# Optimization experiments

Hardware: AMD Instinct MI355X
Metric: run time of the kernel (lower is better)

## Reference

```python
import jax, jax.numpy as jnp
import numpy as np
import math


def _fft_size(n: int) -> int:
    return max(2 * 2 ** int(math.ceil(math.log2(n))), 16)


def setup_inputs() -> dict:
    key = jax.random.key(0)
    k1, k2 = jax.random.split(key)
    b, n, d = 4, 8192, 512
    x = jax.random.normal(k1, (b, n, d), dtype=jnp.float32)
    t = jax.random.normal(k2, (n, d), dtype=jnp.float32)
    return {"x": x, "t": t}


def reference(x, t):
    # x: (b, n, d); t: (n, d) Toeplitz coefficients t0..t_{n-1} per channel.
    # o[b, i, d] = gelu( sum_{j<=i} t[i-j, d] * x[b, j, d] )
    # computed via zero-padded real FFT of size >= 2n (causal linear conv).
    b, n, d = x.shape
    N = _fft_size(n)  # 2 * next_pow2(n)
    t_f = jnp.fft.rfft(t, n=N, axis=0)          # (N//2+1, d) complex
    x_f = jnp.fft.rfft(x, n=N, axis=1)          # (b, N//2+1, d) complex
    y = jnp.fft.irfft(x_f * t_f[None], n=N, axis=1)[:, :n, :]  # (b, n, d)
    return jax.nn.gelu(y)
```

## Files before the change

kernel.cpp:

```cpp
#include <hip/hip_runtime.h>
#include <hip/hip_bf16.h>

typedef short short8 __attribute__((ext_vector_type(8)));
typedef float f32x4  __attribute__((ext_vector_type(4)));

#define N_SEQ 8192
#define D_CH  512

constexpr int XSLOTS  = 2048;
constexpr int XLDS_B  = XSLOTS * 8;
constexpr int TSTRIDE = 272;
constexpr int TLDS_B  = 8 * TSTRIDE;
constexpr int ALL_LDS = XLDS_B + TLDS_B;

__device__ __forceinline__ unsigned short f32_to_bf16_bits(float f) {
    union { float f; unsigned int u; } v; v.f = f;
    unsigned int u = v.u;
    unsigned int r = u + 0x7FFFu + ((u >> 16) & 1u);
    return (unsigned short)(r >> 16);
}

__device__ __forceinline__ float gelu_f(float v) {
  float w = v * (2.3022031f + 0.10294296f * v * v);
  float e = __builtin_amdgcn_exp2f(w);
  float r = __builtin_amdgcn_rcpf(e + 1.0f);
  return v - v * r;
}

__global__ __launch_bounds__(256) void transpose_cast_kernel(
    const float* __restrict__ x, const float* __restrict__ t,
    unsigned short* __restrict__ xT, unsigned short* __restrict__ tT) {
  __shared__ float tile[64][65];
  int blk = blockIdx.x;
  int bat = blk >> 10;
  int rem = blk & 1023;
  int i0 = (rem >> 3) << 6;
  int d0 = (rem & 7) << 6;
  const float* src; unsigned short* dst;
  if (bat < 4) { src = x + (size_t)bat * N_SEQ * D_CH; dst = xT + (size_t)bat * D_CH * N_SEQ; }
  else         { src = t;                              dst = tT; }
  int tx = threadIdx.x & 63, ty = threadIdx.x >> 6;
  #pragma unroll
  for (int r = ty; r < 64; r += 4)
    tile[r][tx] = src[(size_t)(i0 + r) * D_CH + (d0 + tx)];
  __syncthreads();
  #pragma unroll
  for (int r = ty; r < 64; r += 4)
    dst[(size_t)(d0 + r) * N_SEQ + (i0 + tx)] = f32_to_bf16_bits(tile[tx][r]);
}

__global__ __launch_bounds__(256) void transpose_out_kernel(
    const float* __restrict__ src, float* __restrict__ dst) {
  __shared__ float tile[64][65];
  int blk = blockIdx.x;
  int b   = blk >> 10;
  int rem = blk & 1023;
  int d0 = (rem & 7) << 6;
  int i0 = (rem >> 3) << 6;
  int tx = threadIdx.x & 63, ty = threadIdx.x >> 6;
  #pragma unroll
  for (int r = ty; r < 64; r += 4)
    tile[r][tx] = src[((size_t)(d0 + r) * 4 + b) * N_SEQ + i0 + tx];
  __syncthreads();
  #pragma unroll
  for (int r = ty; r < 64; r += 4)
    dst[((size_t)b * N_SEQ + i0 + r) * D_CH + d0 + tx] = tile[tx][r];
}

template<int DMAJOR>
__global__ __launch_bounds__(64) void tno_conv_kernel(
    const unsigned short* __restrict__ xT, const unsigned short* __restrict__ tT,
    float* __restrict__ outp) {
  __shared__ __align__(16) char lds[ALL_LDS];
  const int lane = threadIdx.x & 63;
  const int blk  = blockIdx.x;
  const int d    = blk & 511;
  const int pr   = blk >> 9;

  const int m      = lane & 15;
  const int kb     = (lane >> 4) << 3;
  const int bcol   = m & 3;
  const int sl     = m >> 2;
  const int rA     = m & 7;
  const int aConst = kb - (m & 8);
  char* ldsX = lds;
  char* ldsT = lds + XLDS_B;
  const char* tb = ldsT + rA * TSTRIDE;
  const int stJ  = lane & 31;
  const int stR0 = (lane >> 5) << 2;
  const unsigned short* tTd = tT + ((size_t)d << 13);
  const int uLin = (lane & 3) | ((lane >> 4) << 2);
  const int sb   = (lane >> 2) & 3;
  const unsigned short* xlaneB = xT + (((size_t)sb * D_CH + d) << 13) + (uLin << 1);

  typedef __attribute__((address_space(3))) unsigned int lds_u32;
  typedef const __attribute__((address_space(1))) unsigned int glb_u32;

  #pragma unroll 1
  for (int si = 0; si < 2; ++si) {
    const int strip = si ? (7 - pr) : pr;
    const int base  = strip << 10;
    const int l_hi  = base + 960;

    f32x4 acc[4][4];
    #pragma unroll
    for (int g = 0; g < 4; ++g)
      #pragma unroll
      for (int k = 0; k < 4; ++k)
        acc[g][k] = (f32x4){0.f, 0.f, 0.f, 0.f};

    asm volatile("s_waitcnt vmcnt(0)" ::: "memory");

    unsigned short tp0 = tTd[l_hi + 32 + stJ];
    unsigned short tp1 = tTd[l_hi + stJ];
    unsigned short tp2 = tTd[l_hi - 32 + stJ];
    asm volatile("" ::: "memory");

    #pragma unroll
    for (int j = 0; j < 30; ++j) {
      int by = (1088 + 32 * j) << 3;
      *(unsigned int*)(ldsX + by + (lane << 2)) = 0u;
    }
    #pragma unroll
    for (int j = 0; j < 9; ++j) {
      int R = 32 * j;
      __builtin_amdgcn_global_load_lds((glb_u32*)(xlaneB + R),
                                       (lds_u32*)(ldsX + (R << 3)), 4, 0, 0);
    }
    asm volatile("" ::: "memory");

    #pragma unroll
    for (int c = 0; c < 4; ++c) {
      int r = stR0 + c;
      char* cw = ldsT + r * TSTRIDE;
      *(unsigned short*)(cw + (((r - (l_hi + 32 + stJ)) & 127) << 1)) = tp0;
      *(unsigned short*)(cw + (((r - (l_hi      + stJ)) & 127) << 1)) = tp1;
      *(unsigned short*)(cw + (((r - (l_hi - 32 + stJ)) & 127) << 1)) = tp2;
    }

    unsigned short tv[8];
    #pragma unroll
    for (int u = 0; u < 8; ++u)
      tv[u] = tTd[l_hi - 32 * u - 63 + stJ];

    int aC = ((aConst - l_hi) & 127) << 1;
    short8 af2 = *(const short8*)(tb + ((aC - 64) & 255));
    short8 af3 = *(const short8*)(tb + ((aC - 96) & 255));
    int xo[4];
    #pragma unroll
    for (int g = 0; g < 4; ++g)
      xo[g] = ((((base + ((((g << 2) + sl) << 6) + kb) - l_hi) & 2047) << 3) | (bcol << 4));
    int twb[4];
    #pragma unroll
    for (int c = 0; c < 4; ++c)
      twb[c] = (((stR0 + c) - (l_hi - 63 + stJ)) & 127) << 1;
    int tgi = l_hi - 319 + stJ;
    const unsigned short* xsp = xlaneB + 288;
    int wb = 288 << 3;

#define CONV_ITER(GMIN, U)                                                       \
  {                                                                              \
    asm volatile("s_waitcnt vmcnt(14)" ::: "memory");                            \
    short8 af0 = *(const short8*)(tb + aC);                                      \
    short8 af1 = *(const short8*)(tb + ((aC - 32) & 255));                       \
    __builtin_amdgcn_global_load_lds((glb_u32*)xsp, (lds_u32*)(ldsX + wb), 4, 0, 0); \
    __builtin_amdgcn_s_setprio(1);                                               \
    _Pragma("unroll")                                                            \
    for (int g = 0; g < 4; ++g) {                                                \
      if (g >= (GMIN)) {                                                         \
        short8 bf = *(const short8*)(ldsX + xo[g]);                              \
        acc[g][0] = __builtin_amdgcn_mfma_f32_16x16x32_bf16(af0, bf, acc[g][0], 0, 0, 0); \
        acc[g][1] = __builtin_amdgcn_mfma_f32_16x16x32_bf16(af1, bf, acc[g][1], 0, 0, 0); \
        acc[g][2] = __builtin_amdgcn_mfma_f32_16x16x32_bf16(af2, bf, acc[g][2], 0, 0, 0); \
        acc[g][3] = __builtin_amdgcn_mfma_f32_16x16x32_bf16(af3, bf, acc[g][3], 0, 0, 0); \
      }                                                                          \
      xo[g] = (xo[g] + 256) & 16383;                                             \
    }                                                                            \
    __builtin_amdgcn_s_setprio(0);                                               \
    { unsigned short tvs = tv[U];                                                \
      _Pragma("unroll")                                                          \
      for (int c = 0; c < 4; ++c) {                                              \
        *(unsigned short*)(ldsT + (stR0 + c) * TSTRIDE + twb[c]) = tvs;          \
        twb[c] = (twb[c] + 64) & 255;                                            \
      }                                                                          \
    }                                                                            \
    { unsigned short v = 0;                                                      \
      if (tgi >= 0) v = tTd[tgi];                                                \
      tv[U] = v; tgi -= 32; }                                                    \
    af2 = af0; af3 = af1;                                                        \
    aC = (aC + 64) & 255;                                                        \
    xsp += 32;                                                                   \
    wb = (wb + 256) & 16383;                                                     \
  }

#define PH8(GMIN)                                                                \
    { _Pragma("unroll")                                                          \
      for (int u = 0; u < 8; ++u) CONV_ITER(GMIN, u) }

    PH8(3)
    PH8(2)
    PH8(1)
    const int n0 = (strip << 2) + 1;
    #pragma unroll 1
    for (int c8 = 0; c8 < n0; ++c8)
      PH8(0)
#undef PH8
#undef CONV_ITER

    if (DMAJOR) {
      float* op = outp + ((((size_t)d << 2) + bcol) << 13) + base + (sl << 6) + ((lane >> 4) << 2);
      #pragma unroll
      for (int g = 0; g < 4; ++g)
        #pragma unroll
        for (int k = 0; k < 4; ++k)
          #pragma unroll
          for (int r = 0; r < 4; ++r)
            op[(g << 8) + (k << 4) + r] = gelu_f(acc[g][k][r]);
    } else {
      #pragma unroll
      for (int g = 0; g < 4; ++g)
        #pragma unroll
        for (int k = 0; k < 4; ++k)
          #pragma unroll
          for (int r = 0; r < 4; ++r) {
            int i = base + (((g << 2) + sl) << 6) + (k << 4) + ((lane >> 4) << 2) + r;
            outp[(((size_t)bcol << 13) + (size_t)i) * D_CH + d] = gelu_f(acc[g][k][r]);
          }
    }
  }
}

extern "C" void kernel_launch(void* const* d_in, const int* in_sizes, int n_in,
                              void* d_out, int out_size, void* d_ws, size_t ws_size,
                              hipStream_t stream) {
  const float* x = (const float*)d_in[0];
  const float* t = (const float*)d_in[1];
  float* out = (float*)d_out;

  const size_t xT_elems = (size_t)4 * D_CH * N_SEQ;
  const size_t tT_elems = (size_t)D_CH * N_SEQ;
  unsigned short* xT = (unsigned short*)d_ws;
  unsigned short* tT = xT + xT_elems;
  float* ows = (float*)(tT + tT_elems);
  const size_t need = xT_elems * 2 + tT_elems * 2 + (size_t)4 * N_SEQ * D_CH * 4;
  const bool dmaj = (ws_size >= need);

  hipLaunchKernelGGL(transpose_cast_kernel, dim3(5 * 1024), dim3(256), 0, stream,
                     x, t, xT, tT);
  if (dmaj) {
    hipLaunchKernelGGL((tno_conv_kernel<1>), dim3(2048), dim3(64), 0, stream,
                       xT, tT, ows);
    hipLaunchKernelGGL(transpose_out_kernel, dim3(4096), dim3(256), 0, stream,
                       ows, out);
  } else {
    hipLaunchKernelGGL((tno_conv_kernel<0>), dim3(2048), dim3(64), 0, stream,
                       xT, tT, out);
  }
}
```

Before: 202.3 us.

## Split strip pairs into separate blocks and shrink LDS ring for occupancy

```diff
diff --git a/kernel.cpp b/kernel.cpp
--- a/kernel.cpp
+++ b/kernel.cpp
@@ -7,7 +7,7 @@
 #define N_SEQ 8192
 #define D_CH  512
 
-constexpr int XSLOTS  = 2048;
+constexpr int XSLOTS  = 1280;
 constexpr int XLDS_B  = XSLOTS * 8;
 constexpr int TSTRIDE = 272;
 constexpr int TLDS_B  = 8 * TSTRIDE;
@@ -68,14 +68,16 @@
 }
 
 template<int DMAJOR>
-__global__ __launch_bounds__(64) void tno_conv_kernel(
+__global__ __launch_bounds__(64, 3) void tno_conv_kernel(
     const unsigned short* __restrict__ xT, const unsigned short* __restrict__ tT,
     float* __restrict__ outp) {
   __shared__ __align__(16) char lds[ALL_LDS];
   const int lane = threadIdx.x & 63;
   const int blk  = blockIdx.x;
   const int d    = blk & 511;
-  const int pr   = blk >> 9;
+  const int strip = 7 - (blk >> 9);
+  const int base  = strip << 10;
+  const int l_hi  = base + 960;
 
   const int m      = lane & 15;
   const int kb     = (lane >> 4) << 3;
@@ -96,74 +98,72 @@
   typedef __attribute__((address_space(3))) unsigned int lds_u32;
   typedef const __attribute__((address_space(1))) unsigned int glb_u32;
 
-  #pragma unroll 1
-  for (int si = 0; si < 2; ++si) {
-    const int strip = si ? (7 - pr) : pr;
-    const int base  = strip << 10;
-    const int l_hi  = base + 960;
-
-    f32x4 acc[4][4];
-    #pragma unroll
-    for (int g = 0; g < 4; ++g)
-      #pragma unroll
-      for (int k = 0; k < 4; ++k)
-        acc[g][k] = (f32x4){0.f, 0.f, 0.f, 0.f};
-
-    asm volatile("s_waitcnt vmcnt(0)" ::: "memory");
-
-    unsigned short tp0 = tTd[l_hi + 32 + stJ];
-    unsigned short tp1 = tTd[l_hi + stJ];
-    unsigned short tp2 = tTd[l_hi - 32 + stJ];
-    asm volatile("" ::: "memory");
-
-    #pragma unroll
-    for (int j = 0; j < 30; ++j) {
-      int by = (1088 + 32 * j) << 3;
-      *(unsigned int*)(ldsX + by + (lane << 2)) = 0u;
-    }
-    #pragma unroll
-    for (int j = 0; j < 9; ++j) {
-      int R = 32 * j;
-      __builtin_amdgcn_global_load_lds((glb_u32*)(xlaneB + R),
-                                       (lds_u32*)(ldsX + (R << 3)), 4, 0, 0);
-    }
-    asm volatile("" ::: "memory");
-
-    #pragma unroll
-    for (int c = 0; c < 4; ++c) {
-      int r = stR0 + c;
-      char* cw = ldsT + r * TSTRIDE;
-      *(unsigned short*)(cw + (((r - (l_hi + 32 + stJ)) & 127) << 1)) = tp0;
-      *(unsigned short*)(cw + (((r - (l_hi      + stJ)) & 127) << 1)) = tp1;
-      *(unsigned short*)(cw + (((r - (l_hi - 32 + stJ)) & 127) << 1)) = tp2;
-    }
-
-    unsigned short tv[8];
-    #pragma unroll
-    for (int u = 0; u < 8; ++u)
-      tv[u] = tTd[l_hi - 32 * u - 63 + stJ];
-
-    int aC = ((aConst - l_hi) & 127) << 1;
-    short8 af2 = *(const short8*)(tb + ((aC - 64) & 255));
-    short8 af3 = *(const short8*)(tb + ((aC - 96) & 255));
-    int xo[4];
-    #pragma unroll
-    for (int g = 0; g < 4; ++g)
-      xo[g] = ((((base + ((((g << 2) + sl) << 6) + kb) - l_hi) & 2047) << 3) | (bcol << 4));
-    int twb[4];
-    #pragma unroll
-    for (int c = 0; c < 4; ++c)
-      twb[c] = (((stR0 + c) - (l_hi - 63 + stJ)) & 127) << 1;
-    int tgi = l_hi - 319 + stJ;
-    const unsigned short* xsp = xlaneB + 288;
-    int wb = 288 << 3;
+  f32x4 acc[4][4];
+  #pragma unroll
+  for (int g = 0; g < 4; ++g)
+    #pragma unroll
+    for (int k = 0; k < 4; ++k)
+      acc[g][k] = (f32x4){0.f, 0.f, 0.f, 0.f};
+
+  unsigned short tp0 = tTd[l_hi + 32 + stJ];
+  unsigned short tp1 = tTd[l_hi + stJ];
+  unsigned short tp2 = tTd[l_hi - 32 + stJ];
+  asm volatile("" ::: "memory");
+
+  {
+    f32x4 z = (f32x4){0.f, 0.f, 0.f, 0.f};
+    #pragma unroll
+    for (int j = 0; j < 7; ++j)
+      *(f32x4*)(ldsX + 2560 + (j << 10) + (lane << 4)) = z;
+    *(unsigned long long*)(ldsX + 9728 + (lane << 3)) = 0ull;
+    #pragma unroll
+    for (int j = 0; j < 8; ++j)
+      __builtin_amdgcn_global_load_lds((glb_u32*)(const void*)(xlaneB + (j << 5)),
+                                       (lds_u32*)(void*)(ldsX + (j << 8)), 4, 0, 0);
+  }
+  asm volatile("" ::: "memory");
+
+  #pragma unroll
+  for (int c = 0; c < 4; ++c) {
+    int r = stR0 + c;
+    char* cw = ldsT + r * TSTRIDE;
+    *(unsigned short*)(cw + (((r - (l_hi + 32 + stJ)) & 127) << 1)) = tp0;
+    *(unsigned short*)(cw + (((r - (l_hi      + stJ)) & 127) << 1)) = tp1;
+    *(unsigned short*)(cw + (((r - (l_hi - 32 + stJ)) & 127) << 1)) = tp2;
+  }
+
+  unsigned short tv[8];
+  #pragma unroll
+  for (int u = 0; u < 8; ++u)
+    tv[u] = tTd[l_hi - 32 * u - 63 + stJ];
+
+  asm volatile("s_waitcnt vmcnt(0)" ::: "memory");
+
+  int aC = ((aConst - l_hi) & 127) << 1;
+  short8 af2 = *(const short8*)(tb + ((aC - 64) & 255));
+  short8 af3 = *(const short8*)(tb + ((aC - 96) & 255));
+  int xo[4];
+  #pragma unroll
+  for (int g = 0; g < 4; ++g) {
+    int row = (base - l_hi) + (g << 8) + (sl << 6) + kb;
+    int slot = row + ((row < 0) ? XSLOTS : 0);
+    xo[g] = (slot << 3) + (bcol << 4);
+  }
+  int twb[4];
+  #pragma unroll
+  for (int c = 0; c < 4; ++c)
+    twb[c] = (((stR0 + c) - (l_hi - 63 + stJ)) & 127) << 1;
+  int tgi = l_hi - 319 + stJ;
+  const unsigned short* xsp = xlaneB + 256;
+  int wb = 256 << 3;
 
 #define CONV_ITER(GMIN, U)                                                       \
   {                                                                              \
     asm volatile("s_waitcnt vmcnt(14)" ::: "memory");                            \
     short8 af0 = *(const short8*)(tb + aC);                                      \
     short8 af1 = *(const short8*)(tb + ((aC - 32) & 255));                       \
-    __builtin_amdgcn_global_load_lds((glb_u32*)xsp, (lds_u32*)(ldsX + wb), 4, 0, 0); \
+    __builtin_amdgcn_global_load_lds((glb_u32*)(const void*)xsp,                 \
+        (lds_u32*)(void*)(ldsX + wb), 4, 0, 0);                                  \
     __builtin_amdgcn_s_setprio(1);                                               \
     _Pragma("unroll")                                                            \
     for (int g = 0; g < 4; ++g) {                                                \
@@ -174,7 +174,7 @@
         acc[g][2] = __builtin_amdgcn_mfma_f32_16x16x32_bf16(af2, bf, acc[g][2], 0, 0, 0); \
         acc[g][3] = __builtin_amdgcn_mfma_f32_16x16x32_bf16(af3, bf, acc[g][3], 0, 0, 0); \
       }                                                                          \
-      xo[g] = (xo[g] + 256) & 16383;                                             \
+      xo[g] += 256; if (xo[g] >= XLDS_B) xo[g] -= XLDS_B;                        \
     }                                                                            \
     __builtin_amdgcn_s_setprio(0);                                               \
     { unsigned short tvs = tv[U];                                                \
@@ -184,49 +184,51 @@
         twb[c] = (twb[c] + 64) & 255;                                            \
       }                                                                          \
     }                                                                            \
-    { unsigned short v = 0;                                                      \
-      if (tgi >= 0) v = tTd[tgi];                                                \
-      tv[U] = v; tgi -= 32; }                                                    \
+    { int ti = (tgi < 0) ? 0 : tgi;                                              \
+      unsigned short v = tTd[ti];               \
+      tv[U] = (tgi < 0) ? (unsigned short)0 : v;                                 \
+      tgi -= 32; }                                                               \
     af2 = af0; af3 = af1;                                                        \
     aC = (aC + 64) & 255;                                                        \
     xsp += 32;                                                                   \
-    wb = (wb + 256) & 16383;                                                     \
+    wb += 256; if (wb >= XLDS_B) wb -= XLDS_B;                                   \
   }
 
 #define PH8(GMIN)                                                                \
     { _Pragma("unroll")                                                          \
       for (int u = 0; u < 8; ++u) CONV_ITER(GMIN, u) }
 
-    PH8(3)
-    PH8(2)
-    PH8(1)
-    const int n0 = (strip << 2) + 1;
-    #pragma unroll 1
-    for (int c8 = 0; c8 < n0; ++c8)
-      PH8(0)
+  PH8(3)
+  PH8(2)
+  PH8(1)
+  const int n0 = (strip << 2) + 1;
+  #pragma unroll 1
+  for (int c8 = 0; c8 < n0; ++c8)
+    PH8(0)
 #undef PH8
 #undef CONV_ITER
 
-    if (DMAJOR) {
-      float* op = outp + ((((size_t)d << 2) + bcol) << 13) + base + (sl << 6) + ((lane >> 4) << 2);
+  asm volatile("s_waitcnt vmcnt(0)" ::: "memory");
+
+  if (DMAJOR) {
+    float* op = outp + ((((size_t)d << 2) + bcol) << 13) + base + (sl << 6) + ((lane >> 4) << 2);
+    #pragma unroll
+    for (int g = 0; g < 4; ++g)
       #pragma unroll
-      for (int g = 0; g < 4; ++g)
+      for (int k = 0; k < 4; ++k)
         #pragma unroll
-        for (int k = 0; k < 4; ++k)
-          #pragma unroll
-          for (int r = 0; r < 4; ++r)
-            op[(g << 8) + (k << 4) + r] = gelu_f(acc[g][k][r]);
-    } else {
+        for (int r = 0; r < 4; ++r)
+          op[(g << 8) + (k << 4) + r] = gelu_f(acc[g][k][r]);
+  } else {
+    #pragma unroll
+    for (int g = 0; g < 4; ++g)
       #pragma unroll
-      for (int g = 0; g < 4; ++g)
+      for (int k = 0; k < 4; ++k)
         #pragma unroll
-        for (int k = 0; k < 4; ++k)
-          #pragma unroll
-          for (int r = 0; r < 4; ++r) {
-            int i = base + (((g << 2) + sl) << 6) + (k << 4) + ((lane >> 4) << 2) + r;
-            outp[(((size_t)bcol << 13) + (size_t)i) * D_CH + d] = gelu_f(acc[g][k][r]);
-          }
-    }
+        for (int r = 0; r < 4; ++r) {
+          int i = base + (((g << 2) + sl) << 6) + (k << 4) + ((lane >> 4) << 2) + r;
+          outp[(((size_t)bcol << 13) + (size_t)i) * D_CH + d] = gelu_f(acc[g][k][r]);
+        }
   }
 }
 
@@ -248,12 +250,12 @@
   hipLaunchKernelGGL(transpose_cast_kernel, dim3(5 * 1024), dim3(256), 0, stream,
                      x, t, xT, tT);
   if (dmaj) {
-    hipLaunchKernelGGL((tno_conv_kernel<1>), dim3(2048), dim3(64), 0, stream,
+    hipLaunchKernelGGL((tno_conv_kernel<1>), dim3(4096), dim3(64), 0, stream,
                        xT, tT, ows);
     hipLaunchKernelGGL(transpose_out_kernel, dim3(4096), dim3(256), 0, stream,
                        ows, out);
   } else {
-    hipLaunchKernelGGL((tno_conv_kernel<0>), dim3(2048), dim3(64), 0, stream,
+    hipLaunchKernelGGL((tno_conv_kernel<0>), dim3(4096), dim3(64), 0, stream,
                        xT, tT, out);
   }
 }
```

Result: faster. 165.9 us (-18.0%).
